# Performance work log

Measured on AMD Instinct MI355X. Metric: run time of the kernel, lower is better.

Reference implementation:

```python
import jax, jax.numpy as jnp
import numpy as np
import math

D = 1024
H = 16
HD = D // H  # 64
SCALE = math.sqrt(HD)


def setup_inputs() -> dict:
    key = jax.random.key(0)
    ks = jax.random.split(key, 4)
    B, S = 2, 2048
    x = jax.random.normal(ks[0], (B, S, D), dtype=jnp.float32)
    attention_mask = jnp.zeros((B, S), dtype=jnp.float32)  # additive mask
    w_attn = jax.random.normal(ks[1], (D, 3 * D), dtype=jnp.float32) * (1.0 / math.sqrt(D))
    b_attn = jnp.zeros((3 * D,), dtype=jnp.float32)
    w_proj = jax.random.normal(ks[2], (D, D), dtype=jnp.float32) * (1.0 / math.sqrt(D))
    b_proj = jnp.zeros((D,), dtype=jnp.float32)
    return {"x": x, "attention_mask": attention_mask, "w_attn": w_attn,
            "b_attn": b_attn, "w_proj": w_proj, "b_proj": b_proj}


def reference(x, attention_mask, w_attn, b_attn, w_proj, b_proj):
    B, S, _ = x.shape
    qkv = x @ w_attn + b_attn                      # [B,S,3D]
    q, k, v = jnp.split(qkv, 3, axis=-1)           # each [B,S,D]
    # split heads -> [B,H,S,HD]
    sh = lambda t: t.reshape(B, S, H, HD).transpose(0, 2, 1, 3)
    q, k, v = sh(q), sh(k), sh(v)
    scores = jnp.einsum('bhqd,bhkd->bhqk', q, k) / SCALE   # [B,H,S,S]
    scores = scores + attention_mask[:, None, None, :]      # additive mask [B,1,1,S]
    attn = jax.nn.softmax(scores, axis=-1)                  # dropout disabled (eval)
    out = jnp.einsum('bhqk,bhkd->bhqd', attn, v)            # [B,H,S,HD]
    out = out.transpose(0, 2, 1, 3).reshape(B, S, D)        # merge heads
    out = out @ w_proj + b_proj                              # resid dropout disabled
    return out
```

## Files before the change

### kernel.cpp

```cpp
#include <hip/hip_runtime.h>
#include <math.h>

#define B_  2
#define S_  2048
#define D_  1024
#define H_  16
#define HD_ 64
#define BS_ (B_ * S_)

typedef float f32x4 __attribute__((ext_vector_type(4)));
typedef int   i32x4 __attribute__((ext_vector_type(4)));

__device__ __forceinline__ float bf2f(unsigned short u) {
    union { unsigned int i; float f; } c; c.i = ((unsigned int)u) << 16; return c.f;
}
__device__ __forceinline__ unsigned short f2bf(float f) {
    union { float f; unsigned int i; } c; c.f = f;
    unsigned int r = c.i + 0x7FFFu + ((c.i >> 16) & 1u);
    return (unsigned short)(r >> 16);
}
__device__ __forceinline__ unsigned int cvtpk_bf16(float lo, float hi) {
    unsigned int r;
    asm volatile("v_cvt_pk_bf16_f32 %0, %1, %2" : "=v"(r) : "v"(lo), "v"(hi));
    return r;
}
__device__ __forceinline__ void gl_lds16(const void* g, void* l) {
    __builtin_amdgcn_global_load_lds((const __attribute__((address_space(1))) void*)g,
                                     (__attribute__((address_space(3))) void*)l, 16, 0, 0);
}
__device__ __forceinline__ void mfma_bf16(f32x4& d, i32x4 a, i32x4 b) {
    asm volatile("v_mfma_f32_16x16x32_bf16 %0, %1, %2, %0" : "+v"(d) : "v"(a), "v"(b));
}

__global__ __launch_bounds__(256) void convert_f32_bf16(
    const float* __restrict__ in, unsigned short* __restrict__ out, int n)
{
    const int i = (blockIdx.x * 256 + threadIdx.x) * 8;
    if (i >= n) return;
    const float4 a = *reinterpret_cast<const float4*>(in + i);
    const float4 b = *reinterpret_cast<const float4*>(in + i + 4);
    ushort4 u0 = make_ushort4(f2bf(a.x), f2bf(a.y), f2bf(a.z), f2bf(a.w));
    ushort4 u1 = make_ushort4(f2bf(b.x), f2bf(b.y), f2bf(b.z), f2bf(b.w));
    *reinterpret_cast<ushort4*>(out + i)     = u0;
    *reinterpret_cast<ushort4*>(out + i + 4) = u1;
}

__global__ __launch_bounds__(256) void transpose_cvt(
    const float* __restrict__ W, unsigned short* __restrict__ Wt, int K, int N)
{
    __shared__ float t[32][33];
    const int n0 = blockIdx.x * 32, k0 = blockIdx.y * 32;
    const int tx = threadIdx.x & 31, ty = threadIdx.x >> 5;
#pragma unroll
    for (int r = 0; r < 32; r += 8)
        t[ty + r][tx] = W[(size_t)(k0 + ty + r) * N + n0 + tx];
    __syncthreads();
#pragma unroll
    for (int r = 0; r < 32; r += 8)
        Wt[(size_t)(n0 + ty + r) * K + k0 + tx] = f2bf(t[tx][ty + r]);
}

template <typename OutT, int BN>
__global__ __launch_bounds__(256) void gemm_bt_bf16(
    const unsigned short* __restrict__ A,
    const unsigned short* __restrict__ Bt,
    const float* __restrict__ bias,
    OutT* __restrict__ C, int M, int N, int K)
{
    constexpr int NW = BN / 2;
    constexpr int NI = NW / 16;
    __shared__ alignas(16) unsigned short As[2][4096];
    __shared__ alignas(16) unsigned short Bs[2][BN * 32];

    const int tid  = threadIdx.x;
    const int wave = tid >> 6;
    const int l    = tid & 63;
    const int g    = l >> 4;
    const int r    = l & 15;
    const int wr   = wave >> 1, wc = wave & 1;
    const int row0 = blockIdx.y * 128;
    const int col0 = blockIdx.x * BN;

    const size_t aoff0 = (size_t)(row0 +   0 + l) * K + wave * 8;
    const size_t aoff1 = (size_t)(row0 +  64 + l) * K + wave * 8;
    const size_t boff0 = (size_t)(col0 +   0 + l) * K + wave * 8;
    const size_t boff1 = (size_t)(col0 +  64 + l) * K + wave * 8;

    auto stage = [&](int kt, int buf) {
        gl_lds16(A + aoff0 + kt, &As[buf][wave * 1024]);
        gl_lds16(A + aoff1 + kt, &As[buf][wave * 1024 + 512]);
        if constexpr (BN == 128) {
            gl_lds16(Bt + boff0 + kt, &Bs[buf][wave * 1024]);
            gl_lds16(Bt + boff1 + kt, &Bs[buf][wave * 1024 + 512]);
        } else {
            gl_lds16(Bt + boff0 + kt, &Bs[buf][wave * 512]);
        }
    };

    f32x4 acc[4][NI];
#pragma unroll
    for (int mi = 0; mi < 4; ++mi)
#pragma unroll
        for (int ni = 0; ni < NI; ++ni) acc[mi][ni] = (f32x4)0.f;

    stage(0, 0);
    __syncthreads();

    for (int kt = 0; kt < K; kt += 32) {
        const int cur = (kt >> 5) & 1;
        if (kt + 32 < K) stage(kt + 32, cur ^ 1);

        const unsigned short* Ab = &As[cur][g * 1024];
        const unsigned short* Bb = &Bs[cur][g * (BN * 8)];
        i32x4 af[4], bf[NI];
#pragma unroll
        for (int mi = 0; mi < 4; ++mi)
            af[mi] = *reinterpret_cast<const i32x4*>(Ab + (wr * 64 + mi * 16 + r) * 8);
#pragma unroll
        for (int ni = 0; ni < NI; ++ni)
            bf[ni] = *reinterpret_cast<const i32x4*>(Bb + (wc * NW + ni * 16 + r) * 8);
#pragma unroll
        for (int mi = 0; mi < 4; ++mi)
#pragma unroll
            for (int ni = 0; ni < NI; ++ni)
                mfma_bf16(acc[mi][ni], af[mi], bf[ni]);

        __syncthreads();
    }

#pragma unroll
    for (int ni = 0; ni < NI; ++ni) {
        const int n = col0 + wc * NW + ni * 16 + r;
        const float bv = bias[n];
#pragma unroll
        for (int mi = 0; mi < 4; ++mi) {
#pragma unroll
            for (int e = 0; e < 4; ++e) {
                const int m = row0 + wr * 64 + mi * 16 + g * 4 + e;
                const float val = acc[mi][ni][e] + bv;
                if constexpr (sizeof(OutT) == 2)
                    C[(size_t)m * N + n] = (OutT)f2bf(val);
                else
                    C[(size_t)m * N + n] = (OutT)val;
            }
        }
    }
}

__global__ __launch_bounds__(512) void flash_attn_mfma(
    const unsigned short* __restrict__ qkv,
    const float* __restrict__ mask,
    unsigned short* __restrict__ out)
{
    __shared__ alignas(16) unsigned short Klds[2][4096];
    __shared__ alignas(16) unsigned short Vt[2][4096];

    const int tid  = threadIdx.x;
    const int wave = tid >> 6;
    const int l    = tid & 63;
    const int g    = l >> 4;
    const int r    = l & 15;
    const int b    = blockIdx.z;
    const int h    = blockIdx.y;
    const int q0   = blockIdx.x * 128;
    const int qw   = q0 + wave * 16;

    const size_t rs = 3 * (size_t)D_;
    const unsigned short* qb = qkv + (size_t)b * S_ * rs + (size_t)h * HD_;
    const unsigned short* kb = qb + D_;
    const unsigned short* vb = qb + 2 * D_;
    const float* mrow = mask + (size_t)b * S_;

    i32x4 qf[2];
#pragma unroll
    for (int ks = 0; ks < 2; ++ks)
        qf[ks] = *reinterpret_cast<const i32x4*>(
            qb + (size_t)(qw + r) * rs + ks * 32 + g * 8);

    const int kkey = (wave & 3) * 16 + (l >> 3);
    const int kuni = ((l & 7) ^ (l >> 3)) * 8;
    const int vkey = (wave & 3) * 16 + (l >> 2);
    const int vpart = l & 3;

    auto stage = [&](int kt, int buf) {
        if (wave < 4) {
            gl_lds16(kb + (size_t)(kt + kkey) * rs + kuni,
                     &Klds[buf][(wave & 3) * 1024]);
            gl_lds16(kb + (size_t)(kt + kkey + 8) * rs + kuni,
                     &Klds[buf][(wave & 3) * 1024 + 512]);
        } else {
#pragma unroll
            for (int p = 0; p < 4; ++p) {
                const int d0 = p * 16 + vpart * 4;
                const ushort4 vv = *reinterpret_cast<const ushort4*>(
                    vb + (size_t)(kt + vkey) * rs + d0);
                Vt[buf][(d0 + 0) * 64 + (vkey ^ (((d0 + 0) & 7) << 3))] = vv.x;
                Vt[buf][(d0 + 1) * 64 + (vkey ^ (((d0 + 1) & 7) << 3))] = vv.y;
                Vt[buf][(d0 + 2) * 64 + (vkey ^ (((d0 + 2) & 7) << 3))] = vv.z;
                Vt[buf][(d0 + 3) * 64 + (vkey ^ (((d0 + 3) & 7) << 3))] = vv.w;
            }
        }
    };

    f32x4 acc[4];
    float m_i = -1e30f, l_i = 0.f;
#pragma unroll
    for (int mi = 0; mi < 4; ++mi) acc[mi] = (f32x4)0.f;

    stage(0, 0);
    __syncthreads();

    for (int kt = 0; kt < S_; kt += 64) {
        const int cur = (kt >> 6) & 1;
        if (kt + 64 < S_) stage(kt + 64, cur ^ 1);

        const unsigned short* Kb = Klds[cur];
        const unsigned short* Vb = Vt[cur];

        f32x4 s[4];
#pragma unroll
        for (int mi = 0; mi < 4; ++mi) s[mi] = (f32x4)0.f;
#pragma unroll
        for (int ks = 0; ks < 2; ++ks)
#pragma unroll
            for (int mi = 0; mi < 4; ++mi) {
                const i32x4 kf = *reinterpret_cast<const i32x4*>(
                    Kb + (mi * 16 + r) * 64 + ((ks * 32 + g * 8) ^ ((r & 7) << 3)));
                mfma_bf16(s[mi], kf, qf[ks]);
            }

#pragma unroll
        for (int mi = 0; mi < 4; ++mi) {
            const float4 mk = *reinterpret_cast<const float4*>(
                mrow + kt + mi * 16 + g * 4);
            s[mi][0] = s[mi][0] * 0.125f + mk.x;
            s[mi][1] = s[mi][1] * 0.125f + mk.y;
            s[mi][2] = s[mi][2] * 0.125f + mk.z;
            s[mi][3] = s[mi][3] * 0.125f + mk.w;
        }

        float tmax = -1e30f;
#pragma unroll
        for (int mi = 0; mi < 4; ++mi)
#pragma unroll
            for (int e = 0; e < 4; ++e)
                tmax = fmaxf(tmax, s[mi][e]);
        tmax = fmaxf(tmax, __shfl_xor(tmax, 16));
        tmax = fmaxf(tmax, __shfl_xor(tmax, 32));
        const float mnew = fmaxf(m_i, tmax);
        const float corr = __expf(m_i - mnew);
        m_i = mnew;

        unsigned int pk[4][2];
        float ls = 0.f;
#pragma unroll
        for (int mi = 0; mi < 4; ++mi) {
            const float p0 = __expf(s[mi][0] - mnew);
            const float p1 = __expf(s[mi][1] - mnew);
            const float p2 = __expf(s[mi][2] - mnew);
            const float p3 = __expf(s[mi][3] - mnew);
            ls += (p0 + p1) + (p2 + p3);
            pk[mi][0] = cvtpk_bf16(p0, p1);
            pk[mi][1] = cvtpk_bf16(p2, p3);
        }
        l_i = l_i * corr + ls;
#pragma unroll
        for (int mi = 0; mi < 4; ++mi) acc[mi] *= corr;

#pragma unroll
        for (int ks = 0; ks < 2; ++ks) {
            i32x4 pf;
#pragma unroll
            for (int w = 0; w < 4; ++w) {
                const int src = (((g & 1) * 2 + (w >> 1)) << 4) + r;
                const unsigned int vA = __shfl(pk[2 * ks + 0][w & 1], src);
                const unsigned int vB = __shfl(pk[2 * ks + 1][w & 1], src);
                pf[w] = (int)((g >> 1) ? vB : vA);
            }
#pragma unroll
            for (int mi = 0; mi < 4; ++mi) {
                const i32x4 vf = *reinterpret_cast<const i32x4*>(
                    Vb + (mi * 16 + r) * 64 + ((ks * 32 + g * 8) ^ ((r & 7) << 3)));
                mfma_bf16(acc[mi], vf, pf);
            }
        }

        __syncthreads();
    }

    float lf = l_i;
    lf += __shfl_xor(lf, 16);
    lf += __shfl_xor(lf, 32);
    const float inv = 1.0f / lf;
    const size_t token = (size_t)b * S_ + qw + r;
#pragma unroll
    for (int mi = 0; mi < 4; ++mi) {
        const f32x4 v = acc[mi] * inv;
        uint2 w;
        w.x = cvtpk_bf16(v[0], v[1]);
        w.y = cvtpk_bf16(v[2], v[3]);
        *reinterpret_cast<uint2*>(
            out + token * D_ + h * HD_ + mi * 16 + g * 4) = w;
    }
}

extern "C" void kernel_launch(void* const* d_in, const int* in_sizes, int n_in,
                              void* d_out, int out_size, void* d_ws, size_t ws_size,
                              hipStream_t stream)
{
    const float* x      = (const float*)d_in[0];
    const float* amask  = (const float*)d_in[1];
    const float* w_attn = (const float*)d_in[2];
    const float* b_attn = (const float*)d_in[3];
    const float* w_proj = (const float*)d_in[4];
    const float* b_proj = (const float*)d_in[5];
    float* out = (float*)d_out;

    unsigned short* qkvb  = (unsigned short*)d_ws;
    unsigned short* attnb = qkvb  + (size_t)BS_ * 3 * D_;
    unsigned short* xb    = attnb + (size_t)BS_ * D_;
    unsigned short* wat   = xb    + (size_t)BS_ * D_;
    unsigned short* wpt   = wat   + (size_t)3 * D_ * D_;

    convert_f32_bf16<<<(BS_ * D_) / 2048, 256, 0, stream>>>(x, xb, BS_ * D_);
    transpose_cvt<<<dim3(3 * D_ / 32, D_ / 32), 256, 0, stream>>>(w_attn, wat, D_, 3 * D_);
    transpose_cvt<<<dim3(D_ / 32, D_ / 32), 256, 0, stream>>>(w_proj, wpt, D_, D_);

    gemm_bt_bf16<unsigned short, 128><<<dim3(3 * D_ / 128, BS_ / 128), 256, 0, stream>>>(
        xb, wat, b_attn, qkvb, BS_, 3 * D_, D_);

    flash_attn_mfma<<<dim3(S_ / 128, H_, B_), 512, 0, stream>>>(qkvb, amask, attnb);

    gemm_bt_bf16<float, 128><<<dim3(D_ / 128, BS_ / 128), 256, 0, stream>>>(
        attnb, wpt, b_proj, out, BS_, D_, D_);
}
```

Measured before the change: 182.1 us.

## Double flash-attention key tile, use exp2 with lazy rescale, add MFMA priority hints

```diff
diff --git a/kernel.cpp b/kernel.cpp
--- a/kernel.cpp
+++ b/kernel.cpp
@@ -7,6 +7,9 @@
 #define H_  16
 #define HD_ 64
 #define BS_ (B_ * S_)
+
+#define LOG2E_   1.44269504088896f
+#define CSCALE_  (0.125f * LOG2E_)
 
 typedef float f32x4 __attribute__((ext_vector_type(4)));
 typedef int   i32x4 __attribute__((ext_vector_type(4)));
@@ -45,6 +48,13 @@
     *reinterpret_cast<ushort4*>(out + i + 4) = u1;
 }
 
+__global__ __launch_bounds__(256) void scale_mask(
+    const float* __restrict__ m, float* __restrict__ m2, int n)
+{
+    const int i = blockIdx.x * 256 + threadIdx.x;
+    if (i < n) m2[i] = m[i] * LOG2E_;
+}
+
 __global__ __launch_bounds__(256) void transpose_cvt(
     const float* __restrict__ W, unsigned short* __restrict__ Wt, int K, int N)
 {
@@ -119,11 +129,13 @@
 #pragma unroll
         for (int ni = 0; ni < NI; ++ni)
             bf[ni] = *reinterpret_cast<const i32x4*>(Bb + (wc * NW + ni * 16 + r) * 8);
+        __builtin_amdgcn_s_setprio(1);
 #pragma unroll
         for (int mi = 0; mi < 4; ++mi)
 #pragma unroll
             for (int ni = 0; ni < NI; ++ni)
                 mfma_bf16(acc[mi][ni], af[mi], bf[ni]);
+        __builtin_amdgcn_s_setprio(0);
 
         __syncthreads();
     }
@@ -149,11 +161,11 @@
 
 __global__ __launch_bounds__(512) void flash_attn_mfma(
     const unsigned short* __restrict__ qkv,
-    const float* __restrict__ mask,
+    const float* __restrict__ mask2,
     unsigned short* __restrict__ out)
 {
-    __shared__ alignas(16) unsigned short Klds[2][4096];
-    __shared__ alignas(16) unsigned short Vt[2][4096];
+    __shared__ alignas(16) unsigned short Klds[2][8192];
+    __shared__ alignas(16) unsigned short Vt[2][8192];
 
     const int tid  = threadIdx.x;
     const int wave = tid >> 6;
@@ -169,7 +181,7 @@
     const unsigned short* qb = qkv + (size_t)b * S_ * rs + (size_t)h * HD_;
     const unsigned short* kb = qb + D_;
     const unsigned short* vb = qb + 2 * D_;
-    const float* mrow = mask + (size_t)b * S_;
+    const float* m2row = mask2 + (size_t)b * S_;
 
     i32x4 qf[2];
 #pragma unroll
@@ -184,20 +196,27 @@
 
     auto stage = [&](int kt, int buf) {
         if (wave < 4) {
-            gl_lds16(kb + (size_t)(kt + kkey) * rs + kuni,
-                     &Klds[buf][(wave & 3) * 1024]);
-            gl_lds16(kb + (size_t)(kt + kkey + 8) * rs + kuni,
-                     &Klds[buf][(wave & 3) * 1024 + 512]);
+#pragma unroll
+            for (int hh = 0; hh < 2; ++hh) {
+                gl_lds16(kb + (size_t)(kt + hh * 64 + kkey) * rs + kuni,
+                         &Klds[buf][hh * 4096 + (wave & 3) * 1024]);
+                gl_lds16(kb + (size_t)(kt + hh * 64 + kkey + 8) * rs + kuni,
+                         &Klds[buf][hh * 4096 + (wave & 3) * 1024 + 512]);
+            }
         } else {
 #pragma unroll
-            for (int p = 0; p < 4; ++p) {
-                const int d0 = p * 16 + vpart * 4;
-                const ushort4 vv = *reinterpret_cast<const ushort4*>(
-                    vb + (size_t)(kt + vkey) * rs + d0);
-                Vt[buf][(d0 + 0) * 64 + (vkey ^ (((d0 + 0) & 7) << 3))] = vv.x;
-                Vt[buf][(d0 + 1) * 64 + (vkey ^ (((d0 + 1) & 7) << 3))] = vv.y;
-                Vt[buf][(d0 + 2) * 64 + (vkey ^ (((d0 + 2) & 7) << 3))] = vv.z;
-                Vt[buf][(d0 + 3) * 64 + (vkey ^ (((d0 + 3) & 7) << 3))] = vv.w;
+            for (int hh = 0; hh < 2; ++hh) {
+                const int kcol = hh * 64 + vkey;
+#pragma unroll
+                for (int p = 0; p < 4; ++p) {
+                    const int d0 = p * 16 + vpart * 4;
+                    const ushort4 vv = *reinterpret_cast<const ushort4*>(
+                        vb + (size_t)(kt + kcol) * rs + d0);
+                    Vt[buf][(d0 + 0) * 128 + (kcol ^ (((d0 + 0) & 7) << 3))] = vv.x;
+                    Vt[buf][(d0 + 1) * 128 + (kcol ^ (((d0 + 1) & 7) << 3))] = vv.y;
+                    Vt[buf][(d0 + 2) * 128 + (kcol ^ (((d0 + 2) & 7) << 3))] = vv.z;
+                    Vt[buf][(d0 + 3) * 128 + (kcol ^ (((d0 + 3) & 7) << 3))] = vv.w;
+                }
             }
         }
     };
@@ -210,65 +229,69 @@
     stage(0, 0);
     __syncthreads();
 
-    for (int kt = 0; kt < S_; kt += 64) {
-        const int cur = (kt >> 6) & 1;
-        if (kt + 64 < S_) stage(kt + 64, cur ^ 1);
+    for (int kt = 0; kt < S_; kt += 128) {
+        const int cur = (kt >> 7) & 1;
+        if (kt + 128 < S_) stage(kt + 128, cur ^ 1);
 
         const unsigned short* Kb = Klds[cur];
         const unsigned short* Vb = Vt[cur];
 
-        f32x4 s[4];
-#pragma unroll
-        for (int mi = 0; mi < 4; ++mi) s[mi] = (f32x4)0.f;
+        f32x4 s[8];
+#pragma unroll
+        for (int mi = 0; mi < 8; ++mi) s[mi] = (f32x4)0.f;
+        __builtin_amdgcn_s_setprio(1);
 #pragma unroll
         for (int ks = 0; ks < 2; ++ks)
 #pragma unroll
-            for (int mi = 0; mi < 4; ++mi) {
+            for (int mi = 0; mi < 8; ++mi) {
                 const i32x4 kf = *reinterpret_cast<const i32x4*>(
                     Kb + (mi * 16 + r) * 64 + ((ks * 32 + g * 8) ^ ((r & 7) << 3)));
                 mfma_bf16(s[mi], kf, qf[ks]);
             }
-
-#pragma unroll
-        for (int mi = 0; mi < 4; ++mi) {
+        __builtin_amdgcn_s_setprio(0);
+
+#pragma unroll
+        for (int mi = 0; mi < 8; ++mi) {
             const float4 mk = *reinterpret_cast<const float4*>(
-                mrow + kt + mi * 16 + g * 4);
-            s[mi][0] = s[mi][0] * 0.125f + mk.x;
-            s[mi][1] = s[mi][1] * 0.125f + mk.y;
-            s[mi][2] = s[mi][2] * 0.125f + mk.z;
-            s[mi][3] = s[mi][3] * 0.125f + mk.w;
+                m2row + kt + mi * 16 + g * 4);
+            s[mi][0] = s[mi][0] * CSCALE_ + mk.x;
+            s[mi][1] = s[mi][1] * CSCALE_ + mk.y;
+            s[mi][2] = s[mi][2] * CSCALE_ + mk.z;
+            s[mi][3] = s[mi][3] * CSCALE_ + mk.w;
         }
 
         float tmax = -1e30f;
 #pragma unroll
-        for (int mi = 0; mi < 4; ++mi)
+        for (int mi = 0; mi < 8; ++mi)
 #pragma unroll
             for (int e = 0; e < 4; ++e)
                 tmax = fmaxf(tmax, s[mi][e]);
         tmax = fmaxf(tmax, __shfl_xor(tmax, 16));
         tmax = fmaxf(tmax, __shfl_xor(tmax, 32));
-        const float mnew = fmaxf(m_i, tmax);
-        const float corr = __expf(m_i - mnew);
-        m_i = mnew;
-
-        unsigned int pk[4][2];
+        if (tmax > m_i + 8.f) {
+            const float corr = exp2f(m_i - tmax);
+            l_i *= corr;
+#pragma unroll
+            for (int mi = 0; mi < 4; ++mi) acc[mi] *= corr;
+            m_i = tmax;
+        }
+
+        unsigned int pk[8][2];
         float ls = 0.f;
 #pragma unroll
-        for (int mi = 0; mi < 4; ++mi) {
-            const float p0 = __expf(s[mi][0] - mnew);
-            const float p1 = __expf(s[mi][1] - mnew);
-            const float p2 = __expf(s[mi][2] - mnew);
-            const float p3 = __expf(s[mi][3] - mnew);
+        for (int mi = 0; mi < 8; ++mi) {
+            const float p0 = exp2f(s[mi][0] - m_i);
+            const float p1 = exp2f(s[mi][1] - m_i);
+            const float p2 = exp2f(s[mi][2] - m_i);
+            const float p3 = exp2f(s[mi][3] - m_i);
             ls += (p0 + p1) + (p2 + p3);
             pk[mi][0] = cvtpk_bf16(p0, p1);
             pk[mi][1] = cvtpk_bf16(p2, p3);
         }
-        l_i = l_i * corr + ls;
-#pragma unroll
-        for (int mi = 0; mi < 4; ++mi) acc[mi] *= corr;
-
-#pragma unroll
-        for (int ks = 0; ks < 2; ++ks) {
+        l_i += ls;
+
+#pragma unroll
+        for (int ks = 0; ks < 4; ++ks) {
             i32x4 pf;
 #pragma unroll
             for (int w = 0; w < 4; ++w) {
@@ -277,12 +300,14 @@
                 const unsigned int vB = __shfl(pk[2 * ks + 1][w & 1], src);
                 pf[w] = (int)((g >> 1) ? vB : vA);
             }
+            __builtin_amdgcn_s_setprio(1);
 #pragma unroll
             for (int mi = 0; mi < 4; ++mi) {
                 const i32x4 vf = *reinterpret_cast<const i32x4*>(
-                    Vb + (mi * 16 + r) * 64 + ((ks * 32 + g * 8) ^ ((r & 7) << 3)));
+                    Vb + (mi * 16 + r) * 128 + ((ks * 32 + g * 8) ^ ((r & 7) << 3)));
                 mfma_bf16(acc[mi], vf, pf);
             }
+            __builtin_amdgcn_s_setprio(0);
         }
 
         __syncthreads();
@@ -321,15 +346,17 @@
     unsigned short* xb    = attnb + (size_t)BS_ * D_;
     unsigned short* wat   = xb    + (size_t)BS_ * D_;
     unsigned short* wpt   = wat   + (size_t)3 * D_ * D_;
+    float*          mask2 = (float*)(wpt + (size_t)D_ * D_);
 
     convert_f32_bf16<<<(BS_ * D_) / 2048, 256, 0, stream>>>(x, xb, BS_ * D_);
+    scale_mask<<<BS_ / 256, 256, 0, stream>>>(amask, mask2, BS_);
     transpose_cvt<<<dim3(3 * D_ / 32, D_ / 32), 256, 0, stream>>>(w_attn, wat, D_, 3 * D_);
     transpose_cvt<<<dim3(D_ / 32, D_ / 32), 256, 0, stream>>>(w_proj, wpt, D_, D_);
 
     gemm_bt_bf16<unsigned short, 128><<<dim3(3 * D_ / 128, BS_ / 128), 256, 0, stream>>>(
         xb, wat, b_attn, qkvb, BS_, 3 * D_, D_);
 
-    flash_attn_mfma<<<dim3(S_ / 128, H_, B_), 512, 0, stream>>>(qkvb, amask, attnb);
+    flash_attn_mfma<<<dim3(S_ / 128, H_, B_), 512, 0, stream>>>(qkvb, mask2, attnb);
 
     gemm_bt_bf16<float, 128><<<dim3(D_ / 128, BS_ / 128), 256, 0, stream>>>(
         attnb, wpt, b_proj, out, BS_, D_, D_);
```

After: 231.6 us. 27.2% more time.

## Use exp2 softmax with lazy rescaling and MFMA wave priority in flash attention

Applied to the files above, without the earlier changes.

```diff
diff --git a/kernel.cpp b/kernel.cpp
--- a/kernel.cpp
+++ b/kernel.cpp
@@ -7,6 +7,9 @@
 #define H_  16
 #define HD_ 64
 #define BS_ (B_ * S_)
+
+#define LOG2E_   1.44269504088896f
+#define CSCALE_  (0.125f * LOG2E_)
 
 typedef float f32x4 __attribute__((ext_vector_type(4)));
 typedef int   i32x4 __attribute__((ext_vector_type(4)));
@@ -45,6 +48,13 @@
     *reinterpret_cast<ushort4*>(out + i + 4) = u1;
 }
 
+__global__ __launch_bounds__(256) void scale_mask(
+    const float* __restrict__ m, float* __restrict__ m2, int n)
+{
+    const int i = blockIdx.x * 256 + threadIdx.x;
+    if (i < n) m2[i] = m[i] * LOG2E_;
+}
+
 __global__ __launch_bounds__(256) void transpose_cvt(
     const float* __restrict__ W, unsigned short* __restrict__ Wt, int K, int N)
 {
@@ -149,7 +159,7 @@
 
 __global__ __launch_bounds__(512) void flash_attn_mfma(
     const unsigned short* __restrict__ qkv,
-    const float* __restrict__ mask,
+    const float* __restrict__ mask2,
     unsigned short* __restrict__ out)
 {
     __shared__ alignas(16) unsigned short Klds[2][4096];
@@ -169,7 +179,7 @@
     const unsigned short* qb = qkv + (size_t)b * S_ * rs + (size_t)h * HD_;
     const unsigned short* kb = qb + D_;
     const unsigned short* vb = qb + 2 * D_;
-    const float* mrow = mask + (size_t)b * S_;
+    const float* m2row = mask2 + (size_t)b * S_;
 
     i32x4 qf[2];
 #pragma unroll
@@ -220,6 +230,7 @@
         f32x4 s[4];
 #pragma unroll
         for (int mi = 0; mi < 4; ++mi) s[mi] = (f32x4)0.f;
+        __builtin_amdgcn_s_setprio(1);
 #pragma unroll
         for (int ks = 0; ks < 2; ++ks)
 #pragma unroll
@@ -228,15 +239,16 @@
                     Kb + (mi * 16 + r) * 64 + ((ks * 32 + g * 8) ^ ((r & 7) << 3)));
                 mfma_bf16(s[mi], kf, qf[ks]);
             }
+        __builtin_amdgcn_s_setprio(0);
 
 #pragma unroll
         for (int mi = 0; mi < 4; ++mi) {
             const float4 mk = *reinterpret_cast<const float4*>(
-                mrow + kt + mi * 16 + g * 4);
-            s[mi][0] = s[mi][0] * 0.125f + mk.x;
-            s[mi][1] = s[mi][1] * 0.125f + mk.y;
-            s[mi][2] = s[mi][2] * 0.125f + mk.z;
-            s[mi][3] = s[mi][3] * 0.125f + mk.w;
+                m2row + kt + mi * 16 + g * 4);
+            s[mi][0] = s[mi][0] * CSCALE_ + mk.x;
+            s[mi][1] = s[mi][1] * CSCALE_ + mk.y;
+            s[mi][2] = s[mi][2] * CSCALE_ + mk.z;
+            s[mi][3] = s[mi][3] * CSCALE_ + mk.w;
         }
 
         float tmax = -1e30f;
@@ -247,25 +259,27 @@
                 tmax = fmaxf(tmax, s[mi][e]);
         tmax = fmaxf(tmax, __shfl_xor(tmax, 16));
         tmax = fmaxf(tmax, __shfl_xor(tmax, 32));
-        const float mnew = fmaxf(m_i, tmax);
-        const float corr = __expf(m_i - mnew);
-        m_i = mnew;
+        if (tmax > m_i + 4.f) {
+            const float corr = exp2f(m_i - tmax);
+            l_i *= corr;
+#pragma unroll
+            for (int mi = 0; mi < 4; ++mi) acc[mi] *= corr;
+            m_i = tmax;
+        }
 
         unsigned int pk[4][2];
         float ls = 0.f;
 #pragma unroll
         for (int mi = 0; mi < 4; ++mi) {
-            const float p0 = __expf(s[mi][0] - mnew);
-            const float p1 = __expf(s[mi][1] - mnew);
-            const float p2 = __expf(s[mi][2] - mnew);
-            const float p3 = __expf(s[mi][3] - mnew);
+            const float p0 = exp2f(s[mi][0] - m_i);
+            const float p1 = exp2f(s[mi][1] - m_i);
+            const float p2 = exp2f(s[mi][2] - m_i);
+            const float p3 = exp2f(s[mi][3] - m_i);
             ls += (p0 + p1) + (p2 + p3);
             pk[mi][0] = cvtpk_bf16(p0, p1);
             pk[mi][1] = cvtpk_bf16(p2, p3);
         }
-        l_i = l_i * corr + ls;
-#pragma unroll
-        for (int mi = 0; mi < 4; ++mi) acc[mi] *= corr;
+        l_i += ls;
 
 #pragma unroll
         for (int ks = 0; ks < 2; ++ks) {
@@ -277,12 +291,14 @@
                 const unsigned int vB = __shfl(pk[2 * ks + 1][w & 1], src);
                 pf[w] = (int)((g >> 1) ? vB : vA);
             }
+            __builtin_amdgcn_s_setprio(1);
 #pragma unroll
             for (int mi = 0; mi < 4; ++mi) {
                 const i32x4 vf = *reinterpret_cast<const i32x4*>(
                     Vb + (mi * 16 + r) * 64 + ((ks * 32 + g * 8) ^ ((r & 7) << 3)));
                 mfma_bf16(acc[mi], vf, pf);
             }
+            __builtin_amdgcn_s_setprio(0);
         }
 
         __syncthreads();
@@ -321,15 +337,17 @@
     unsigned short* xb    = attnb + (size_t)BS_ * D_;
     unsigned short* wat   = xb    + (size_t)BS_ * D_;
     unsigned short* wpt   = wat   + (size_t)3 * D_ * D_;
+    float*          mask2 = (float*)(wpt + (size_t)D_ * D_);
 
     convert_f32_bf16<<<(BS_ * D_) / 2048, 256, 0, stream>>>(x, xb, BS_ * D_);
+    scale_mask<<<BS_ / 256, 256, 0, stream>>>(amask, mask2, BS_);
     transpose_cvt<<<dim3(3 * D_ / 32, D_ / 32), 256, 0, stream>>>(w_attn, wat, D_, 3 * D_);
     transpose_cvt<<<dim3(D_ / 32, D_ / 32), 256, 0, stream>>>(w_proj, wpt, D_, D_);
 
     gemm_bt_bf16<unsigned short, 128><<<dim3(3 * D_ / 128, BS_ / 128), 256, 0, stream>>>(
         xb, wat, b_attn, qkvb, BS_, 3 * D_, D_);
 
-    flash_attn_mfma<<<dim3(S_ / 128, H_, B_), 512, 0, stream>>>(qkvb, amask, attnb);
+    flash_attn_mfma<<<dim3(S_ / 128, H_, B_), 512, 0, stream>>>(qkvb, mask2, attnb);
 
     gemm_bt_bf16<float, 128><<<dim3(D_ / 128, BS_ / 128), 256, 0, stream>>>(
         attnb, wpt, b_proj, out, BS_, D_, D_);
```

Result: slower. 186.5 us (+2.5%).
